# Performance work log

Measured on AMD Instinct MI355X. Metric: run time of the kernel, lower is better.

## Reference

```python
import jax, jax.numpy as jnp
import numpy as np

DIM_K = 64
DIM_V = 64
MODEL_DIM = 1024


def setup_inputs() -> dict:
    key = jax.random.key(0)
    ks = jax.random.split(key, 9)
    B, T, C = 4, 4096, MODEL_DIM
    scale = 1.0 / np.sqrt(C)
    return {
        "Q": jax.random.normal(ks[0], (B, T, C), dtype=jnp.float32),
        "K": jax.random.normal(ks[1], (B, T, C), dtype=jnp.float32),
        "V": jax.random.normal(ks[2], (B, T, C), dtype=jnp.float32),
        "Wq": jax.random.normal(ks[3], (C, DIM_K), dtype=jnp.float32) * scale,
        "bq": jax.random.normal(ks[4], (DIM_K,), dtype=jnp.float32) * 0.02,
        "Wk": jax.random.normal(ks[5], (C, DIM_K), dtype=jnp.float32) * scale,
        "bk": jax.random.normal(ks[6], (DIM_K,), dtype=jnp.float32) * 0.02,
        "Wv": jax.random.normal(ks[7], (C, DIM_V), dtype=jnp.float32) * scale,
        "bv": jax.random.normal(ks[8], (DIM_V,), dtype=jnp.float32) * 0.02,
    }


def reference(Q, K, V, Wq, bq, Wk, bk, Wv, bv):
    # Linear projections: [B,T,C] @ [C,dk] -> [B,T,dk]
    q = jnp.einsum("btc,cd->btd", Q, Wq) + bq
    k = jnp.einsum("btc,cd->btd", K, Wk) + bk
    v = jnp.einsum("btc,cd->btd", V, Wv) + bv
    T = q.shape[1]
    # Scaled dot-product scores [B,T,T], causal mask, softmax (dropout p=0 -> identity)
    scores = jnp.einsum("bqd,bkd->bqk", q, k) / jnp.sqrt(jnp.float32(DIM_K))
    causal = jnp.tril(jnp.ones((T, T), dtype=bool))
    scores = jnp.where(causal, scores, -jnp.inf)
    weights = jax.nn.softmax(scores, axis=-1)
    return jnp.einsum("bqk,bkd->bqd", weights, v)
```

## Files before the change

### kernel.cpp

```cpp
#include <hip/hip_runtime.h>
#include <hip/hip_bf16.h>
#include <cstdint>
#include <cstddef>


typedef __attribute__((ext_vector_type(8))) short short8;
typedef __attribute__((ext_vector_type(4))) float f32x4;
typedef __attribute__((ext_vector_type(4))) unsigned int uint4v;
typedef __attribute__((ext_vector_type(4))) unsigned short ushort4v;
typedef unsigned short ushort;

#define MFMA16x16x32(A,B,C) __builtin_amdgcn_mfma_f32_16x16x32_bf16((A),(B),(C),0,0,0)

static __device__ __forceinline__ unsigned pack2_bf16(float f0, float f1){
  unsigned u0 = __builtin_bit_cast(unsigned, f0) + 0x8000u;
  unsigned u1 = __builtin_bit_cast(unsigned, f1) + 0x8000u;
  return __builtin_amdgcn_perm(u1, u0, 0x07060302u);
}
static __device__ __forceinline__ unsigned short bf16u(float f){
  return (unsigned short)((__builtin_bit_cast(unsigned, f) + 0x8000u) >> 16);
}
static __device__ __forceinline__ short8 cvt8(f32x4 a, f32x4 b){
  union { unsigned u[4]; short8 s; } r;
  r.u[0] = pack2_bf16(a[0], a[1]);
  r.u[1] = pack2_bf16(a[2], a[3]);
  r.u[2] = pack2_bf16(b[0], b[1]);
  r.u[3] = pack2_bf16(b[2], b[3]);
  return r.s;
}
static __device__ __forceinline__ float fast_exp2(float x){
  float r; asm("v_exp_f32 %0, %1" : "=v"(r) : "v"(x)); return r;
}
static __device__ __forceinline__ float fast_rcp(float x){
  float r; asm("v_rcp_f32 %0, %1" : "=v"(r) : "v"(x)); return r;
}
static __device__ __forceinline__ void gl_lds16(const ushort* g, ushort* l){
  __builtin_amdgcn_global_load_lds(
      (const __attribute__((address_space(1))) void*)g,
      (__attribute__((address_space(3))) void*)l, 16, 0, 0);
}

__global__ __launch_bounds__(256) void pack_w(
    const float* __restrict__ Wq, const float* __restrict__ Wk,
    const float* __restrict__ Wv, unsigned short* __restrict__ Wp,
    float* __restrict__ out, float* __restrict__ Lbuf)
{
  int t = blockIdx.x * 256 + threadIdx.x;
  if (t < 24576){
    int lane = t & 63, nf = (t >> 6) & 3, cc = (t >> 8) & 31, p = t >> 13;
    int qd = lane >> 4, l = lane & 15;
    const float* W = (p == 0) ? Wq : ((p == 1) ? Wk : Wv);
    const float* src = W + (size_t)(cc * 32 + qd * 8) * 64 + nf * 16 + l;
    uint4v u;
    #pragma unroll
    for (int j = 0; j < 4; ++j)
      u[j] = pack2_bf16(src[(2 * j) * 64], src[(2 * j + 1) * 64]);
    *(uint4v*)(Wp + (size_t)t * 8) = u;
  }
  const f32x4 z = (f32x4){0.f, 0.f, 0.f, 0.f};
  f32x4* o4 = (f32x4*)out;
  f32x4* l4 = (f32x4*)Lbuf;
  for (int i = t; i < 262144 + 4096; i += 65536){
    if (i < 262144) o4[i] = z;
    else l4[i - 262144] = z;
  }
}

__global__ __launch_bounds__(256) void proj_gemm(
    const float* __restrict__ Qx, const float* __restrict__ Kx, const float* __restrict__ Vx,
    const float* __restrict__ bqp, const float* __restrict__ bkp, const float* __restrict__ bvp,
    const unsigned short* __restrict__ Wp,
    unsigned short* __restrict__ qb, unsigned short* __restrict__ kb,
    unsigned short* __restrict__ vt)
{
  const int tid = threadIdx.x;
  const int lane = tid & 63, wid = tid >> 6;
  const int qd = lane >> 4, l = lane & 15;
  const int p = blockIdx.y;
  const float* X = (p == 0) ? Qx : ((p == 1) ? Kx : Vx);
  const float* bias = (p == 0) ? bqp : ((p == 1) ? bkp : bvp);
  const unsigned short* W = Wp + (size_t)p * 65536;

  const int row0 = blockIdx.x * 64 + wid * 16;
  const float* xa = X + (size_t)(row0 + l) * 1024 + qd * 8;
  const unsigned short* wb = W + (size_t)lane * 8;

  f32x4 acc[4];
  #pragma unroll
  for (int nf = 0; nf < 4; ++nf) acc[nf] = (f32x4){0.f, 0.f, 0.f, 0.f};

  #pragma unroll 4
  for (int cc = 0; cc < 32; ++cc){
    f32x4 al = *(const f32x4*)(xa + cc * 32);
    f32x4 ah = *(const f32x4*)(xa + cc * 32 + 4);
    const unsigned short* wc = wb + (size_t)cc * 2048;
    short8 b0 = *(const short8*)(wc);
    short8 b1 = *(const short8*)(wc + 512);
    short8 b2 = *(const short8*)(wc + 1024);
    short8 b3 = *(const short8*)(wc + 1536);
    short8 a = cvt8(al, ah);
    acc[0] = MFMA16x16x32(a, b0, acc[0]);
    acc[1] = MFMA16x16x32(a, b1, acc[1]);
    acc[2] = MFMA16x16x32(a, b2, acc[2]);
    acc[3] = MFMA16x16x32(a, b3, acc[3]);
  }

  if (p == 2){
    int tg = row0 + qd * 4;
    int b = tg >> 12, tl = tg & 4095;
    #pragma unroll
    for (int nf = 0; nf < 4; ++nf){
      float bb = bias[nf * 16 + l];
      ushort4v pk;
      #pragma unroll
      for (int r = 0; r < 4; ++r) pk[r] = bf16u(acc[nf][r] + bb);
      *(ushort4v*)(vt + ((size_t)b * 64 + nf * 16 + l) * 4096 + tl) = pk;
    }
  } else {
    unsigned short* o = (p == 0) ? qb : kb;
    #pragma unroll
    for (int nf = 0; nf < 4; ++nf){
      float bb = bias[nf * 16 + l];
      #pragma unroll
      for (int r = 0; r < 4; ++r){
        int row = row0 + qd * 4 + r;
        o[(size_t)row * 64 + nf * 16 + l] = bf16u(acc[nf][r] + bb);
      }
    }
  }
}

#define K1 0.18033688011112042f

__global__ __launch_bounds__(256) void flash_split(
    const ushort* __restrict__ qb, const ushort* __restrict__ kb,
    const ushort* __restrict__ vt, float* __restrict__ out,
    float* __restrict__ Lbuf)
{
  __shared__ ushort Ks[2][4096];
  __shared__ ushort Vs[2][4096];
  __shared__ ushort pbuf[4][16 * 40];

  const int tid = threadIdx.x;
  const int lane = tid & 63, wid = tid >> 6;
  const int qd = lane >> 4, l = lane & 15;
  const int lw = l & 7;

  int bidx = (int)blockIdx.x;
  const int batch = bidx & 3;
  int j = 287 - (bidx >> 2);
  int g = 0;
  while (j >= 4 * (g + 1) * (g + 2)) ++g;
  int j2 = j - 4 * g * (g + 1);
  int tq = j2 / (g + 1);
  int s = j2 - tq * (g + 1);
  const int q0b = (8 * g + tq) * 64;
  const int kvstart = s * 512;
  const int kvend = min(kvstart + 512, q0b + 64);
  const int q0w = q0b + wid * 16;

  const ushort* kbB = kb + (size_t)batch * 262144;
  const ushort* vtB = vt + (size_t)batch * 262144;

  const ushort* qrow = qb + ((size_t)(batch * 4096 + q0w + l)) * 64 + qd * 8;
  short8 Qf0 = *(const short8*)(qrow);
  short8 Qf1 = *(const short8*)(qrow + 32);

  const f32x4 Zc = (f32x4){0.f, 0.f, 0.f, 0.f};
  f32x4 Oc[4] = {Zc, Zc, Zc, Zc};
  f32x4 Lacc = Zc;
  short8 onesf;
  #pragma unroll
  for (int i = 0; i < 8; ++i) onesf[i] = (short)0x3F80;

  ushort* pw = &pbuf[wid][0];
  ushort* pwr = pw + qd * 160 + l;
  const ushort* prd = pw + l * 40 + qd * 8;

#define STAGE(BB, KVC) do{                                                     \
    int r8_ = lane >> 3, sw_ = ((lane & 7) ^ r8_) << 3;                        \
    int rA_ = wid * 8 + r8_;                                                   \
    const ushort* gk_ = kbB + (size_t)((KVC) + rA_) * 64 + sw_;                \
    gl_lds16(gk_,            &Ks[BB][wid * 512]);                              \
    gl_lds16(gk_ + 32 * 64,  &Ks[BB][2048 + wid * 512]);                       \
    const ushort* gv_ = vtB + (size_t)rA_ * 4096 + (KVC) + sw_;                \
    gl_lds16(gv_,              &Vs[BB][wid * 512]);                            \
    gl_lds16(gv_ + 32 * 4096,  &Vs[BB][2048 + wid * 512]);                     \
  } while (0)

#define CHUNK(BB, ROFF, KVG) do{                                               \
    if ((KVG) < q0w + 16){                                                     \
      const ushort* KsB_ = &Ks[BB][0];                                         \
      const ushort* VsB_ = &Vs[BB][0];                                         \
      short8 k0_ = *(const short8*)(KsB_ + (l + (ROFF)) * 64 + ((qd ^ lw) << 3));        \
      short8 k1_ = *(const short8*)(KsB_ + (l + (ROFF)) * 64 + (((qd + 4) ^ lw) << 3));  \
      short8 k2_ = *(const short8*)(KsB_ + (l + 16 + (ROFF)) * 64 + ((qd ^ lw) << 3));   \
      short8 k3_ = *(const short8*)(KsB_ + (l + 16 + (ROFF)) * 64 + (((qd + 4) ^ lw) << 3)); \
      f32x4 s0_ = MFMA16x16x32(Qf0, k0_, Zc);                                  \
      s0_ = MFMA16x16x32(Qf1, k1_, s0_);                                       \
      f32x4 s1_ = MFMA16x16x32(Qf0, k2_, Zc);                                  \
      s1_ = MFMA16x16x32(Qf1, k3_, s1_);                                       \
      float p0_[4], p1_[4];                                                    \
      _Pragma("unroll")                                                        \
      for (int r = 0; r < 4; ++r){                                             \
        p0_[r] = fast_exp2(s0_[r] * K1);                                       \
        p1_[r] = fast_exp2(s1_[r] * K1);                                       \
      }                                                                        \
      if ((KVG) + 31 > q0w){                                                   \
        _Pragma("unroll")                                                      \
        for (int r = 0; r < 4; ++r){                                           \
          int q_ = q0w + qd * 4 + r;                                           \
          if ((KVG) + l > q_) p0_[r] = 0.f;                                    \
          if ((KVG) + 16 + l > q_) p1_[r] = 0.f;                               \
        }                                                                      \
      }                                                                        \
      _Pragma("unroll")                                                        \
      for (int r = 0; r < 4; ++r){                                             \
        pwr[r * 40] = bf16u(p0_[r]);                                           \
        pwr[r * 40 + 16] = bf16u(p1_[r]);                                      \
      }                                                                        \
      short8 Pf_ = *(const short8*)(prd);                                      \
      int vs_ = ((qd + ((ROFF) >> 3)) ^ lw) << 3;                              \
      short8 v0_ = *(const short8*)(VsB_ + (l     ) * 64 + vs_);               \
      short8 v1_ = *(const short8*)(VsB_ + (l + 16) * 64 + vs_);               \
      short8 v2_ = *(const short8*)(VsB_ + (l + 32) * 64 + vs_);               \
      short8 v3_ = *(const short8*)(VsB_ + (l + 48) * 64 + vs_);               \
      Lacc = MFMA16x16x32(Pf_, onesf, Lacc);                                   \
      Oc[0] = MFMA16x16x32(Pf_, v0_, Oc[0]);                                   \
      Oc[1] = MFMA16x16x32(Pf_, v1_, Oc[1]);                                   \
      Oc[2] = MFMA16x16x32(Pf_, v2_, Oc[2]);                                   \
      Oc[3] = MFMA16x16x32(Pf_, v3_, Oc[3]);                                   \
    }                                                                          \
  } while (0)

  const int nst = (kvend - kvstart) >> 6;
  STAGE(0, kvstart);
  __syncthreads();
  int kvc = kvstart;
  for (int it = 0; it < nst; ++it){
    int bb = it & 1;
    if (it + 1 < nst) STAGE(bb ^ 1, kvc + 64);
    CHUNK(bb, 0, kvc);
    CHUNK(bb, 32, kvc + 32);
    __syncthreads();
    kvc += 64;
  }
#undef STAGE
#undef CHUNK

  float* ob = out + ((size_t)(batch * 4096 + q0w + qd * 4)) * 64 + l;
  #pragma unroll
  for (int nf = 0; nf < 4; ++nf)
    #pragma unroll
    for (int r = 0; r < 4; ++r)
      atomicAdd(&ob[(size_t)r * 64 + nf * 16], Oc[nf][r]);
  if (l == 0){
    float* lb = Lbuf + batch * 4096 + q0w + qd * 4;
    #pragma unroll
    for (int r = 0; r < 4; ++r) atomicAdd(&lb[r], Lacc[r]);
  }
}

__global__ __launch_bounds__(256) void normalize(
    float* __restrict__ out, const float* __restrict__ Lbuf)
{
  int idx = blockIdx.x * 256 + threadIdx.x;
  f32x4 v = ((f32x4*)out)[idx];
  float inv = fast_rcp(Lbuf[idx >> 4]);
  v[0] *= inv; v[1] *= inv; v[2] *= inv; v[3] *= inv;
  ((f32x4*)out)[idx] = v;
}

extern "C" void kernel_launch(void* const* d_in, const int* in_sizes, int n_in,
                              void* d_out, int out_size, void* d_ws, size_t ws_size,
                              hipStream_t stream)
{
  const float* Q  = (const float*)d_in[0];
  const float* K  = (const float*)d_in[1];
  const float* V  = (const float*)d_in[2];
  const float* Wq = (const float*)d_in[3];
  const float* bq = (const float*)d_in[4];
  const float* Wk = (const float*)d_in[5];
  const float* bk = (const float*)d_in[6];
  const float* Wv = (const float*)d_in[7];
  const float* bv = (const float*)d_in[8];
  float* out = (float*)d_out;

  unsigned short* qb   = (unsigned short*)d_ws;
  unsigned short* kbuf = qb + (size_t)16384 * 64;
  unsigned short* vtp  = kbuf + (size_t)16384 * 64;
  unsigned short* Wp   = vtp + (size_t)16384 * 64;
  float* Lbuf = (float*)(Wp + (size_t)3 * 65536);

  pack_w<<<256, 256, 0, stream>>>(Wq, Wk, Wv, Wp, out, Lbuf);
  proj_gemm<<<dim3(256, 3), 256, 0, stream>>>(Q, K, V, bq, bk, bv, Wp, qb, kbuf, vtp);
  flash_split<<<1152, 256, 0, stream>>>(qb, kbuf, vtp, out, Lbuf);
  normalize<<<1024, 256, 0, stream>>>(out, Lbuf);
}
```

Measured before the change: 253.1 us.

## Stage projection inputs through double-buffered swizzled LDS via global_load_lds

The projection GEMM now stages each 64-row by 64-column fp32 slice of X into shared memory with async global-to-LDS loads, double-buffered, before converting to bf16 for MFMA. The next slice is fetched while the current one is computed on. An XOR swizzle on the 16-byte column chunks is meant to avoid LDS bank conflicts on the per-lane reads. The aim is better-coalesced, latency-hidden reads of the large fp32 input, at the cost of 32KB of LDS per block and a barrier on every stage.

```diff
diff --git a/kernel.cpp b/kernel.cpp
--- a/kernel.cpp
+++ b/kernel.cpp
@@ -34,7 +34,7 @@
 static __device__ __forceinline__ float fast_rcp(float x){
   float r; asm("v_rcp_f32 %0, %1" : "=v"(r) : "v"(x)); return r;
 }
-static __device__ __forceinline__ void gl_lds16(const ushort* g, ushort* l){
+static __device__ __forceinline__ void gl_lds16(const void* g, void* l){
   __builtin_amdgcn_global_load_lds(
       (const __attribute__((address_space(1))) void*)g,
       (__attribute__((address_space(3))) void*)l, 16, 0, 0);
@@ -73,6 +73,7 @@
     unsigned short* __restrict__ qb, unsigned short* __restrict__ kb,
     unsigned short* __restrict__ vt)
 {
+  __shared__ float Xs[2][4096];
   const int tid = threadIdx.x;
   const int lane = tid & 63, wid = tid >> 6;
   const int qd = lane >> 4, l = lane & 15;
@@ -81,32 +82,60 @@
   const float* bias = (p == 0) ? bqp : ((p == 1) ? bkp : bvp);
   const unsigned short* W = Wp + (size_t)p * 65536;
 
-  const int row0 = blockIdx.x * 64 + wid * 16;
-  const float* xa = X + (size_t)(row0 + l) * 1024 + qd * 8;
+  const int row0 = blockIdx.x * 64;
   const unsigned short* wb = W + (size_t)lane * 8;
+
+  const int rloc16 = 4 * wid + qd;
+  const int jsw = l ^ rloc16;
+  const float* gsrc = X + (size_t)(row0 + rloc16) * 1024 + jsw * 4;
+
+#define STAGE(BB, ST) do{                                                      \
+    const float* g_ = gsrc + (ST) * 64;                                        \
+    float* d_ = &Xs[BB][wid * 256];                                            \
+    gl_lds16(g_,               d_);                                            \
+    gl_lds16(g_ + 16 * 1024,   d_ + 1024);                                     \
+    gl_lds16(g_ + 32 * 1024,   d_ + 2048);                                     \
+    gl_lds16(g_ + 48 * 1024,   d_ + 3072);                                     \
+  } while (0)
 
   f32x4 acc[4];
   #pragma unroll
   for (int nf = 0; nf < 4; ++nf) acc[nf] = (f32x4){0.f, 0.f, 0.f, 0.f};
 
-  #pragma unroll 4
-  for (int cc = 0; cc < 32; ++cc){
-    f32x4 al = *(const f32x4*)(xa + cc * 32);
-    f32x4 ah = *(const f32x4*)(xa + cc * 32 + 4);
-    const unsigned short* wc = wb + (size_t)cc * 2048;
-    short8 b0 = *(const short8*)(wc);
-    short8 b1 = *(const short8*)(wc + 512);
-    short8 b2 = *(const short8*)(wc + 1024);
-    short8 b3 = *(const short8*)(wc + 1536);
-    short8 a = cvt8(al, ah);
-    acc[0] = MFMA16x16x32(a, b0, acc[0]);
-    acc[1] = MFMA16x16x32(a, b1, acc[1]);
-    acc[2] = MFMA16x16x32(a, b2, acc[2]);
-    acc[3] = MFMA16x16x32(a, b3, acc[3]);
-  }
-
+  const int rloc = wid * 16 + l;
+  const float* xrow0 = &Xs[0][rloc * 64];
+  const float* xrow1 = &Xs[1][rloc * 64];
+
+  STAGE(0, 0);
+  __syncthreads();
+  #pragma unroll 2
+  for (int st = 0; st < 16; ++st){
+    int bb = st & 1;
+    if (st + 1 < 16) STAGE(bb ^ 1, st + 1);
+    const float* xr = bb ? xrow1 : xrow0;
+    #pragma unroll
+    for (int kc = 0; kc < 2; ++kc){
+      int j0 = kc * 8 + 2 * qd;
+      f32x4 al = *(const f32x4*)(xr + ((j0 ^ l) << 2));
+      f32x4 ah = *(const f32x4*)(xr + (((j0 + 1) ^ l) << 2));
+      const unsigned short* wc = wb + (size_t)(st * 2 + kc) * 2048;
+      short8 b0 = *(const short8*)(wc);
+      short8 b1 = *(const short8*)(wc + 512);
+      short8 b2 = *(const short8*)(wc + 1024);
+      short8 b3 = *(const short8*)(wc + 1536);
+      short8 a = cvt8(al, ah);
+      acc[0] = MFMA16x16x32(a, b0, acc[0]);
+      acc[1] = MFMA16x16x32(a, b1, acc[1]);
+      acc[2] = MFMA16x16x32(a, b2, acc[2]);
+      acc[3] = MFMA16x16x32(a, b3, acc[3]);
+    }
+    __syncthreads();
+  }
+#undef STAGE
+
+  const int rw0 = row0 + wid * 16;
   if (p == 2){
-    int tg = row0 + qd * 4;
+    int tg = rw0 + qd * 4;
     int b = tg >> 12, tl = tg & 4095;
     #pragma unroll
     for (int nf = 0; nf < 4; ++nf){
@@ -123,7 +152,7 @@
       float bb = bias[nf * 16 + l];
       #pragma unroll
       for (int r = 0; r < 4; ++r){
-        int row = row0 + qd * 4 + r;
+        int row = rw0 + qd * 4 + r;
         o[(size_t)row * 64 + nf * 16 + l] = bf16u(acc[nf][r] + bb);
       }
     }
```

New measurement: 262.4 us. 1.04x slower.

## Split projection GEMM over K across waves with LDS staging and reduction

Applied to the files above, without the earlier changes.

The projection kernel now processes 16 rows per block and splits the 1024-wide reduction across the four waves. It stages the fp32 input tile into LDS via global_load_lds with an XOR swizzle, then reduces the per-wave partial results through LDS before adding bias and writing with vectorized stores. The grid grows from 256 to 1024 blocks per projection, which should give more parallelism and coalesced, memory-bound loads. In exchange it uses 64KB of LDS per block, which limits occupancy, and adds two barriers and an LDS reduction.

```diff
diff --git a/kernel.cpp b/kernel.cpp
--- a/kernel.cpp
+++ b/kernel.cpp
@@ -34,7 +34,7 @@
 static __device__ __forceinline__ float fast_rcp(float x){
   float r; asm("v_rcp_f32 %0, %1" : "=v"(r) : "v"(x)); return r;
 }
-static __device__ __forceinline__ void gl_lds16(const ushort* g, ushort* l){
+static __device__ __forceinline__ void gl_lds16(const void* g, void* l){
   __builtin_amdgcn_global_load_lds(
       (const __attribute__((address_space(1))) void*)g,
       (__attribute__((address_space(3))) void*)l, 16, 0, 0);
@@ -73,27 +73,40 @@
     unsigned short* __restrict__ qb, unsigned short* __restrict__ kb,
     unsigned short* __restrict__ vt)
 {
+  __shared__ float Xs[4][4096];
   const int tid = threadIdx.x;
   const int lane = tid & 63, wid = tid >> 6;
   const int qd = lane >> 4, l = lane & 15;
   const int p = blockIdx.y;
   const float* X = (p == 0) ? Qx : ((p == 1) ? Kx : Vx);
   const float* bias = (p == 0) ? bqp : ((p == 1) ? bkp : bvp);
-  const unsigned short* W = Wp + (size_t)p * 65536;
-
-  const int row0 = blockIdx.x * 64 + wid * 16;
-  const float* xa = X + (size_t)(row0 + l) * 1024 + qd * 8;
-  const unsigned short* wb = W + (size_t)lane * 8;
+  const ushort* W = Wp + (size_t)p * 65536;
+
+  const int rowg = blockIdx.x * 16;
+  float* xw = &Xs[wid][0];
+
+  {
+    const float* gbase = X + (size_t)rowg * 1024 + wid * 256;
+    #pragma unroll
+    for (int r = 0; r < 16; ++r){
+      const float* g = gbase + (size_t)r * 1024 + ((lane ^ (r & 7)) << 2);
+      gl_lds16(g, xw + r * 256);
+    }
+  }
+  __syncthreads();
 
   f32x4 acc[4];
   #pragma unroll
   for (int nf = 0; nf < 4; ++nf) acc[nf] = (f32x4){0.f, 0.f, 0.f, 0.f};
 
-  #pragma unroll 4
-  for (int cc = 0; cc < 32; ++cc){
-    f32x4 al = *(const f32x4*)(xa + cc * 32);
-    f32x4 ah = *(const f32x4*)(xa + cc * 32 + 4);
-    const unsigned short* wc = wb + (size_t)cc * 2048;
+  const float* xrow = xw + l * 256;
+  const ushort* wbase = W + (size_t)(wid * 8) * 2048 + lane * 8;
+  #pragma unroll
+  for (int kc = 0; kc < 8; ++kc){
+    int c0 = kc * 8 + qd * 2;
+    f32x4 al = *(const f32x4*)(xrow + ((c0 ^ (l & 7)) << 2));
+    f32x4 ah = *(const f32x4*)(xrow + (((c0 + 1) ^ (l & 7)) << 2));
+    const ushort* wc = wbase + (size_t)kc * 2048;
     short8 b0 = *(const short8*)(wc);
     short8 b1 = *(const short8*)(wc + 512);
     short8 b2 = *(const short8*)(wc + 1024);
@@ -105,28 +118,36 @@
     acc[3] = MFMA16x16x32(a, b3, acc[3]);
   }
 
+  #pragma unroll
+  for (int nf = 0; nf < 4; ++nf)
+    #pragma unroll
+    for (int r = 0; r < 4; ++r)
+      xw[(qd * 4 + r) * 64 + nf * 16 + l] = acc[nf][r];
+  __syncthreads();
+
   if (p == 2){
-    int tg = row0 + qd * 4;
-    int b = tg >> 12, tl = tg & 4095;
-    #pragma unroll
-    for (int nf = 0; nf < 4; ++nf){
-      float bb = bias[nf * 16 + l];
-      ushort4v pk;
-      #pragma unroll
-      for (int r = 0; r < 4; ++r) pk[r] = bf16u(acc[nf][r] + bb);
-      *(ushort4v*)(vt + ((size_t)b * 64 + nf * 16 + l) * 4096 + tl) = pk;
+    int col = tid & 63, r0 = (tid >> 6) << 2;
+    float bb = bias[col];
+    ushort4v pk;
+    #pragma unroll
+    for (int r = 0; r < 4; ++r){
+      int o = (r0 + r) * 64 + col;
+      float s = Xs[0][o] + Xs[1][o] + Xs[2][o] + Xs[3][o];
+      pk[r] = bf16u(s + bb);
     }
+    int b = rowg >> 12, tl = rowg & 4095;
+    *(ushort4v*)(vt + ((size_t)b * 64 + col) * 4096 + tl + r0) = pk;
   } else {
-    unsigned short* o = (p == 0) ? qb : kb;
-    #pragma unroll
-    for (int nf = 0; nf < 4; ++nf){
-      float bb = bias[nf * 16 + l];
-      #pragma unroll
-      for (int r = 0; r < 4; ++r){
-        int row = row0 + qd * 4 + r;
-        o[(size_t)row * 64 + nf * 16 + l] = bf16u(acc[nf][r] + bb);
-      }
+    ushort* o = (p == 0) ? qb : kb;
+    int row = tid >> 4, col0 = (tid & 15) << 2;
+    ushort4v pk;
+    #pragma unroll
+    for (int c = 0; c < 4; ++c){
+      int off = row * 64 + col0 + c;
+      float s = Xs[0][off] + Xs[1][off] + Xs[2][off] + Xs[3][off];
+      pk[c] = bf16u(s + bias[col0 + c]);
     }
+    *(ushort4v*)(o + (size_t)(rowg + row) * 64 + col0) = pk;
   }
 }
 
@@ -293,7 +314,7 @@
   float* Lbuf = (float*)(Wp + (size_t)3 * 65536);
 
   pack_w<<<256, 256, 0, stream>>>(Wq, Wk, Wv, Wp, out, Lbuf);
-  proj_gemm<<<dim3(256, 3), 256, 0, stream>>>(Q, K, V, bq, bk, bv, Wp, qb, kbuf, vtp);
+  proj_gemm<<<dim3(1024, 3), 256, 0, stream>>>(Q, K, V, bq, bk, bv, Wp, qb, kbuf, vtp);
   flash_split<<<1152, 256, 0, stream>>>(qb, kbuf, vtp, out, Lbuf);
   normalize<<<1024, 256, 0, stream>>>(out, Lbuf);
 }
```

New measurement: 257.0 us. About the same (+1.5%).
